# Optimization experiments

Measured on AMD Instinct MI355X. Metric: run time of the kernel, lower is better.

Reference implementation:

```python
import jax, jax.numpy as jnp
import numpy as np

B, N, D = 8, 2048, 128

def setup_inputs() -> dict:
    key = jax.random.key(0)
    k1, k2, k3 = jax.random.split(key, 3)
    embeddings = jax.random.normal(k1, (B, N, D), dtype=jnp.float32)
    cost_matrix = jax.random.uniform(k2, (B, N, N), dtype=jnp.float32)
    W = jax.random.normal(k3, (D, 2 * D), dtype=jnp.float32) * (1.0 / np.sqrt(2 * D))
    b = jnp.zeros((D,), dtype=jnp.float32)
    return {"embeddings": embeddings, "cost_matrix": cost_matrix, "W": W, "b": b}

def reference(embeddings, cost_matrix, W, b):
    # degree[b,j] = number of nonzero entries in row j of cost_matrix
    degree = (cost_matrix != 0).astype(embeddings.dtype).sum(axis=-1)  # [B,N]
    # sum_neighbors[b,j,d] = sum_i embeddings[b,i,d] * cost_matrix[b,i,j]
    # (algebraic rewrite of the O(B*N*N*D) broadcast-multiply-reduce)
    sum_neighbors = jnp.einsum('bij,bid->bjd', cost_matrix, embeddings)
    sum_neighbors = sum_neighbors / degree[..., None]
    concatenated = jnp.concatenate([embeddings, sum_neighbors], axis=-1)  # [B,N,2D]
    return jax.nn.relu(jnp.einsum('bnf,df->bnd', concatenated, W) + b)
```

## Files before the change

kernel.cpp:

```cpp
#include <hip/hip_runtime.h>
#include <stdint.h>

#define B_ 8
#define N_ 2048
#define D_ 128
#define KS_ 4
#define KT_ 8
#define PS_ ((size_t)B_ * N_ * D_)

typedef unsigned short u16;
typedef unsigned int u32;
using f32x4 = __attribute__((ext_vector_type(4))) float;
using bf16x8 = __attribute__((ext_vector_type(8))) short;
using u16x8 = __attribute__((ext_vector_type(8))) u16;

__device__ inline u16 f2bf(float x) {
  u32 u = __float_as_uint(x);
  return (u16)((u + 0x7FFFu + ((u >> 16) & 1u)) >> 16);
}
__device__ inline float bf2f(u16 h) { return __uint_as_float((u32)h << 16); }

__global__ __launch_bounds__(256) void prep_et_kernel(const float* __restrict__ E,
                                                      u16* __restrict__ ET) {
  __shared__ float Els[64][132];
  const int blk = blockIdx.x;
  const int b = blk >> 5;
  const int i0 = (blk & 31) * 64;
  const int t = threadIdx.x;
  const float* Eb = E + ((size_t)b * N_ + i0) * D_;
#pragma unroll
  for (int s = 0; s < 8; ++s) {
    const int r = (t >> 5) + 8 * s;
    const int c = t & 31;
    f32x4 v = *(const f32x4*)(Eb + r * D_ + c * 4);
#pragma unroll
    for (int e = 0; e < 4; ++e) Els[r][c * 4 + e] = v[e];
  }
  __syncthreads();
  u16* ETb = ET + (size_t)b * D_ * N_;
#pragma unroll
  for (int s = 0; s < 4; ++s) {
    const int d = (t >> 3) + 32 * s;
    const int g = t & 7;
    u16x8 pk;
#pragma unroll
    for (int e = 0; e < 8; ++e) pk[e] = f2bf(Els[g * 8 + e][d]);
    *(u16x8*)(ETb + (size_t)d * N_ + i0 + g * 8) = pk;
  }
}

__global__ __launch_bounds__(256) void gemm_kernel(const float* __restrict__ C,
                                                   const u16* __restrict__ ET,
                                                   u16* __restrict__ Sp,
                                                   int* __restrict__ deg) {
  __shared__ __align__(16) u16 Asw[64 * 64];
  __shared__ __align__(16) u16 Bsw[128 * 64];
  const int phys = blockIdx.x;
  const int orig = (phys & 7) * 128 + (phys >> 3);
  const int b = orig >> 7;
  const int ks = (orig >> 5) & 3;
  const int jt = orig & 31;
  const int j0 = jt * 64;
  const int t = threadIdx.x;
  const int lane = t & 63;
  const int wave = t >> 6;
  const int wm = wave >> 1, wn = wave & 1;
  const int lm = lane & 15, lh = lane >> 4;

  const float* Cb = C + (size_t)b * N_ * N_;
  const u16* ETb = ET + (size_t)b * D_ * N_;
  u16* Sb = Sp + (size_t)ks * PS_ + ((size_t)b * N_ + j0) * D_;
  int* degb = deg + b * N_;

  f32x4 acc[2][4];
#pragma unroll
  for (int i = 0; i < 2; ++i)
#pragma unroll
    for (int j = 0; j < 4; ++j) acc[i][j] = (f32x4)0.0f;

  const int aRow = t >> 4, aCol = t & 15;
  const int bG = t & 7;
  const int kbase = ks * (N_ / KS_);

  f32x4 av[4];
  u16x8 bv[4];
#pragma unroll
  for (int s = 0; s < 4; ++s)
    av[s] = *(const f32x4*)(Cb + (size_t)(kbase + aRow + 16 * s) * N_ + j0 + aCol * 4);
#pragma unroll
  for (int s = 0; s < 4; ++s) {
    const int d = (t >> 3) + 32 * s;
    bv[s] = *(const u16x8*)(ETb + (size_t)d * N_ + kbase + bG * 8);
  }

#pragma unroll
  for (int kt = 0; kt < KT_; ++kt) {
    const int i0 = kbase + kt * 64;
#pragma unroll
    for (int s = 0; s < 4; ++s) {
      const int d = (t >> 3) + 32 * s;
      const int swz = (d ^ (d >> 3)) & 7;
      *(u16x8*)&Bsw[d * 64 + ((bG ^ swz) << 3)] = bv[s];
    }
#pragma unroll
    for (int s = 0; s < 4; ++s) {
      const int i = aRow + 16 * s;
      f32x4 v = av[s];
      int cnt = (v[0] != 0.0f) + (v[1] != 0.0f) + (v[2] != 0.0f) + (v[3] != 0.0f);
      cnt += __shfl_xor(cnt, 1);
      cnt += __shfl_xor(cnt, 2);
      cnt += __shfl_xor(cnt, 4);
      cnt += __shfl_xor(cnt, 8);
      if ((lane & 15) == 0) atomicAdd(&degb[i0 + i], cnt);
#pragma unroll
      for (int e = 0; e < 4; ++e) {
        const int jl = aCol * 4 + e;
        const int swz = (jl ^ (jl >> 3)) & 7;
        Asw[jl * 64 + (i ^ (swz << 3))] = f2bf(v[e]);
      }
    }
    if (kt + 1 < KT_) {
      const int i0n = i0 + 64;
#pragma unroll
      for (int s = 0; s < 4; ++s)
        av[s] = *(const f32x4*)(Cb + (size_t)(i0n + aRow + 16 * s) * N_ + j0 + aCol * 4);
#pragma unroll
      for (int s = 0; s < 4; ++s) {
        const int d = (t >> 3) + 32 * s;
        bv[s] = *(const u16x8*)(ETb + (size_t)d * N_ + i0n + bG * 8);
      }
    }
    asm volatile("s_waitcnt lgkmcnt(0)" ::: "memory");
    __builtin_amdgcn_sched_barrier(0);
    __builtin_amdgcn_s_barrier();
    __builtin_amdgcn_sched_barrier(0);
    bf16x8 af[2][2], bfr[4][2];
#pragma unroll
    for (int fm = 0; fm < 2; ++fm) {
      const int jl = wm * 32 + fm * 16 + lm;
      const int swz = (jl ^ (jl >> 3)) & 7;
#pragma unroll
      for (int kf = 0; kf < 2; ++kf) {
        const int K8 = kf * 32 + lh * 8;
        af[fm][kf] = *(const bf16x8*)&Asw[jl * 64 + (K8 ^ (swz << 3))];
      }
    }
#pragma unroll
    for (int fn = 0; fn < 4; ++fn) {
      const int nl = wn * 64 + fn * 16 + lm;
      const int swz = (nl ^ (nl >> 3)) & 7;
#pragma unroll
      for (int kf = 0; kf < 2; ++kf) {
        const int K8 = kf * 32 + lh * 8;
        bfr[fn][kf] = *(const bf16x8*)&Bsw[nl * 64 + (K8 ^ (swz << 3))];
      }
    }
#pragma unroll
    for (int kf = 0; kf < 2; ++kf)
#pragma unroll
      for (int fm = 0; fm < 2; ++fm)
#pragma unroll
        for (int fn = 0; fn < 4; ++fn)
          acc[fm][fn] = __builtin_amdgcn_mfma_f32_16x16x32_bf16(
              af[fm][kf], bfr[fn][kf], acc[fm][fn], 0, 0, 0);
    __builtin_amdgcn_sched_barrier(0);
    __builtin_amdgcn_s_barrier();
    __builtin_amdgcn_sched_barrier(0);
  }
#pragma unroll
  for (int fm = 0; fm < 2; ++fm)
#pragma unroll
    for (int fn = 0; fn < 4; ++fn)
#pragma unroll
      for (int r = 0; r < 4; ++r) {
        const int row = wm * 32 + fm * 16 + lh * 4 + r;
        const int col = wn * 64 + fn * 16 + lm;
        Sb[(size_t)row * D_ + col] = f2bf(acc[fm][fn][r]);
      }
}

__global__ __launch_bounds__(256) void out_kernel(const float* __restrict__ E,
                                                  const u16* __restrict__ Sp,
                                                  const int* __restrict__ deg,
                                                  const float* __restrict__ W,
                                                  const float* __restrict__ bias,
                                                  float* __restrict__ out) {
  __shared__ __align__(16) u16 Wls[128 * 256];
  __shared__ __align__(16) u16 Als[32 * 256];
  const int r0 = blockIdx.x * 32;
  const int t = threadIdx.x;
  const int lane = t & 63;
  const int wave = t >> 6;
  const int lm = lane & 15, lh = lane >> 4;

  {
    const int d = t >> 1;
    const int swz = (d ^ (d >> 3)) & 7;
    const float* Wd = W + d * 256 + (t & 1) * 128;
    const int k8base = (t & 1) * 16;
#pragma unroll
    for (int s = 0; s < 16; ++s) {
      f32x4 v0 = *(const f32x4*)(Wd + s * 8);
      f32x4 v1 = *(const f32x4*)(Wd + s * 8 + 4);
      u16x8 pk;
#pragma unroll
      for (int e = 0; e < 4; ++e) { pk[e] = f2bf(v0[e]); pk[4 + e] = f2bf(v1[e]); }
      *(u16x8*)&Wls[d * 256 + (((k8base + s) ^ swz) << 3)] = pk;
    }
  }
  {
    const int r = t >> 3;
    const int g = t & 7;
    const int swz = (r ^ (r >> 3)) & 7;
    const float idg = 1.0f / (float)deg[r0 + r];
    const float* Er = E + (size_t)(r0 + r) * D_;
#pragma unroll
    for (int h = 0; h < 2; ++h) {
      const int k8 = g + 8 * h;
      f32x4 v0 = *(const f32x4*)(Er + k8 * 8);
      f32x4 v1 = *(const f32x4*)(Er + k8 * 8 + 4);
      u16x8 pk;
#pragma unroll
      for (int e = 0; e < 4; ++e) { pk[e] = f2bf(v0[e]); pk[4 + e] = f2bf(v1[e]); }
      *(u16x8*)&Als[r * 256 + ((k8 ^ swz) << 3)] = pk;
    }
    const size_t off = (size_t)(r0 + r) * D_;
#pragma unroll
    for (int h = 0; h < 2; ++h) {
      const int kq = g + 8 * h;
      u16x8 p0 = *(const u16x8*)(Sp + 0 * PS_ + off + kq * 8);
      u16x8 p1 = *(const u16x8*)(Sp + 1 * PS_ + off + kq * 8);
      u16x8 p2 = *(const u16x8*)(Sp + 2 * PS_ + off + kq * 8);
      u16x8 p3 = *(const u16x8*)(Sp + 3 * PS_ + off + kq * 8);
      u16x8 pk;
#pragma unroll
      for (int e = 0; e < 8; ++e) {
        float s = (bf2f(p0[e]) + bf2f(p1[e])) + (bf2f(p2[e]) + bf2f(p3[e]));
        pk[e] = f2bf(s * idg);
      }
      const int k8 = 16 + kq;
      *(u16x8*)&Als[r * 256 + ((k8 ^ swz) << 3)] = pk;
    }
  }
  __syncthreads();
  f32x4 acc[2][2];
#pragma unroll
  for (int i = 0; i < 2; ++i)
#pragma unroll
    for (int j = 0; j < 2; ++j) acc[i][j] = (f32x4)0.0f;
  const int dbase = wave * 32;
#pragma unroll
  for (int kf = 0; kf < 8; ++kf) {
    bf16x8 af[2], bfr[2];
#pragma unroll
    for (int fm = 0; fm < 2; ++fm) {
      const int r = fm * 16 + lm;
      const int swz = (r ^ (r >> 3)) & 7;
      af[fm] = *(const bf16x8*)&Als[r * 256 + (((kf * 4 + lh) ^ swz) << 3)];
    }
#pragma unroll
    for (int fn = 0; fn < 2; ++fn) {
      const int d = dbase + fn * 16 + lm;
      const int swz = (d ^ (d >> 3)) & 7;
      bfr[fn] = *(const bf16x8*)&Wls[d * 256 + (((kf * 4 + lh) ^ swz) << 3)];
    }
#pragma unroll
    for (int fm = 0; fm < 2; ++fm)
#pragma unroll
      for (int fn = 0; fn < 2; ++fn)
        acc[fm][fn] = __builtin_amdgcn_mfma_f32_16x16x32_bf16(af[fm], bfr[fn],
                                                              acc[fm][fn], 0, 0, 0);
  }
  float bb[2] = {bias[dbase + lm], bias[dbase + 16 + lm]};
#pragma unroll
  for (int fm = 0; fm < 2; ++fm)
#pragma unroll
    for (int fn = 0; fn < 2; ++fn)
#pragma unroll
      for (int r = 0; r < 4; ++r) {
        const int row = r0 + fm * 16 + lh * 4 + r;
        const int d = dbase + fn * 16 + lm;
        float x = acc[fm][fn][r] + bb[fn];
        out[(size_t)row * D_ + d] = x > 0.0f ? x : 0.0f;
      }
}

extern "C" void kernel_launch(void* const* d_in, const int* in_sizes, int n_in,
                              void* d_out, int out_size, void* d_ws, size_t ws_size,
                              hipStream_t stream) {
  (void)in_sizes; (void)n_in; (void)out_size; (void)ws_size;
  const float* E = (const float*)d_in[0];
  const float* C = (const float*)d_in[1];
  const float* W = (const float*)d_in[2];
  const float* bias = (const float*)d_in[3];
  float* out = (float*)d_out;

  int* deg = (int*)d_ws;
  u16* ET = (u16*)((char*)d_ws + 65536);
  u16* Sp = (u16*)((char*)d_ws + 65536 + 4194304);

  hipMemsetAsync(deg, 0, B_ * N_ * sizeof(int), stream);
  hipLaunchKernelGGL(prep_et_kernel, dim3(256), dim3(256), 0, stream, E, ET);
  hipLaunchKernelGGL(gemm_kernel, dim3(1024), dim3(256), 0, stream, C, ET, Sp, deg);
  hipLaunchKernelGGL(out_kernel, dim3(512), dim3(256), 0, stream, E, Sp, deg, W, bias, out);
}
```

Measured before the change: 230.6 us.

## Double-buffer GEMM with direct global-to-LDS loads of pre-swizzled E tiles

Prep kernel now writes embeddings as pre-swizzled bf16 tile images so the GEMM can copy them straight into LDS with global_load_lds, double-buffered against MFMA work. The K split drops from 4 to 2, halving the grid and the partial-sum traffic the output kernel reduces. W is converted to swizzled bf16 once by a single-block kernel and copied into LDS directly instead of each output block converting it. This trades less occupancy and parallelism in the GEMM for fewer global round trips and better load/compute overlap.

```diff
diff --git a/kernel.cpp b/kernel.cpp
--- a/kernel.cpp
+++ b/kernel.cpp
@@ -4,8 +4,9 @@
 #define B_ 8
 #define N_ 2048
 #define D_ 128
-#define KS_ 4
-#define KT_ 8
+#define NT_ 32
+#define KT_ 16
+#define TILE_BYTES 16384
 #define PS_ ((size_t)B_ * N_ * D_)
 
 typedef unsigned short u16;
@@ -20,45 +21,69 @@
 }
 __device__ inline float bf2f(u16 h) { return __uint_as_float((u32)h << 16); }
 
+__device__ inline void glds16(const void* g, void* l) {
+  __builtin_amdgcn_global_load_lds((const __attribute__((address_space(1))) void*)g,
+                                   (__attribute__((address_space(3))) void*)l, 16, 0, 0);
+}
+
 __global__ __launch_bounds__(256) void prep_et_kernel(const float* __restrict__ E,
-                                                      u16* __restrict__ ET) {
+                                                      u16* __restrict__ ETsw) {
   __shared__ float Els[64][132];
   const int blk = blockIdx.x;
   const int b = blk >> 5;
-  const int i0 = (blk & 31) * 64;
+  const int g = blk & 31;
   const int t = threadIdx.x;
-  const float* Eb = E + ((size_t)b * N_ + i0) * D_;
+  const float* Eb = E + ((size_t)b * N_ + g * 64) * D_;
 #pragma unroll
   for (int s = 0; s < 8; ++s) {
-    const int r = (t >> 5) + 8 * s;
-    const int c = t & 31;
-    f32x4 v = *(const f32x4*)(Eb + r * D_ + c * 4);
-#pragma unroll
-    for (int e = 0; e < 4; ++e) Els[r][c * 4 + e] = v[e];
+    const int f4 = t + 256 * s;
+    const int r = f4 >> 5;
+    const int c4 = f4 & 31;
+    f32x4 v = *(const f32x4*)(Eb + (size_t)r * D_ + c4 * 4);
+#pragma unroll
+    for (int e = 0; e < 4; ++e) Els[r][c4 * 4 + e] = v[e];
   }
   __syncthreads();
-  u16* ETb = ET + (size_t)b * D_ * N_;
-#pragma unroll
-  for (int s = 0; s < 4; ++s) {
-    const int d = (t >> 3) + 32 * s;
-    const int g = t & 7;
+  u16* img = ETsw + ((size_t)b * NT_ + g) * (TILE_BYTES / 2);
+  const int d = t >> 1;
+  const int swz = (d ^ (d >> 3)) & 7;
+#pragma unroll
+  for (int gg = 0; gg < 4; ++gg) {
+    const int grp = (t & 1) * 4 + gg;
     u16x8 pk;
 #pragma unroll
-    for (int e = 0; e < 8; ++e) pk[e] = f2bf(Els[g * 8 + e][d]);
-    *(u16x8*)(ETb + (size_t)d * N_ + i0 + g * 8) = pk;
+    for (int e = 0; e < 8; ++e) pk[e] = f2bf(Els[grp * 8 + e][d]);
+    *(u16x8*)(img + d * 64 + ((grp ^ swz) << 3)) = pk;
+  }
+}
+
+__global__ __launch_bounds__(256) void prep_w_kernel(const float* __restrict__ W,
+                                                     u16* __restrict__ Wsw) {
+  const int t = threadIdx.x;
+  const int d = t >> 1;
+  const int swz = (d ^ (d >> 3)) & 7;
+#pragma unroll
+  for (int s = 0; s < 16; ++s) {
+    const int k8 = (t & 1) * 16 + s;
+    f32x4 v0 = *(const f32x4*)(W + d * 256 + k8 * 8);
+    f32x4 v1 = *(const f32x4*)(W + d * 256 + k8 * 8 + 4);
+    u16x8 pk;
+#pragma unroll
+    for (int e = 0; e < 4; ++e) { pk[e] = f2bf(v0[e]); pk[4 + e] = f2bf(v1[e]); }
+    *(u16x8*)(Wsw + d * 256 + ((k8 ^ swz) << 3)) = pk;
   }
 }
 
 __global__ __launch_bounds__(256) void gemm_kernel(const float* __restrict__ C,
-                                                   const u16* __restrict__ ET,
+                                                   const u16* __restrict__ ETsw,
                                                    u16* __restrict__ Sp,
                                                    int* __restrict__ deg) {
-  __shared__ __align__(16) u16 Asw[64 * 64];
-  __shared__ __align__(16) u16 Bsw[128 * 64];
+  __shared__ __align__(16) u16 Asw[2][64 * 64];
+  __shared__ __align__(16) u16 Bsw[2][128 * 64];
   const int phys = blockIdx.x;
-  const int orig = (phys & 7) * 128 + (phys >> 3);
-  const int b = orig >> 7;
-  const int ks = (orig >> 5) & 3;
+  const int orig = (phys & 7) * 64 + (phys >> 3);
+  const int b = orig >> 6;
+  const int ks = (orig >> 5) & 1;
   const int jt = orig & 31;
   const int j0 = jt * 64;
   const int t = threadIdx.x;
@@ -66,107 +91,106 @@
   const int wave = t >> 6;
   const int wm = wave >> 1, wn = wave & 1;
   const int lm = lane & 15, lh = lane >> 4;
+  const int aRow = t >> 4, aCol = t & 15;
 
   const float* Cb = C + (size_t)b * N_ * N_;
-  const u16* ETb = ET + (size_t)b * D_ * N_;
+  const char* Eimg = (const char*)(ETsw + (size_t)b * NT_ * (TILE_BYTES / 2));
+  int* degb = deg + b * N_;
+  const int g0 = ks * KT_;
+
+  f32x4 acc[2][4];
+#pragma unroll
+  for (int i = 0; i < 2; ++i)
+#pragma unroll
+    for (int j = 0; j < 4; ++j) acc[i][j] = (f32x4)0.0f;
+  f32x4 av[4];
+
+#define ISSUE_B(gi, buf)                                                          \
+  {                                                                               \
+    _Pragma("unroll") for (int s = 0; s < 4; ++s) {                               \
+      const int chunk = s * 4 + wave;                                             \
+      glds16(Eimg + (size_t)(gi)*TILE_BYTES + chunk * 1024 + lane * 16,           \
+             (char*)&Bsw[buf][0] + chunk * 1024);                                 \
+    }                                                                             \
+  }
+#define LOAD_A(gi)                                                                \
+  {                                                                               \
+    _Pragma("unroll") for (int s = 0; s < 4; ++s) av[s] =                         \
+        *(const f32x4*)(Cb + (size_t)((gi)*64 + aRow + 16 * s) * N_ + j0 + aCol * 4); \
+  }
+#define WRITE_A(gi, buf)                                                          \
+  {                                                                               \
+    _Pragma("unroll") for (int s = 0; s < 4; ++s) {                               \
+      const int i = aRow + 16 * s;                                                \
+      f32x4 v = av[s];                                                            \
+      int cnt = (v[0] != 0.0f) + (v[1] != 0.0f) + (v[2] != 0.0f) + (v[3] != 0.0f);\
+      cnt += __shfl_xor(cnt, 1);                                                  \
+      cnt += __shfl_xor(cnt, 2);                                                  \
+      cnt += __shfl_xor(cnt, 4);                                                  \
+      cnt += __shfl_xor(cnt, 8);                                                  \
+      if ((lane & 15) == 0) atomicAdd(&degb[(gi)*64 + i], cnt);                   \
+      _Pragma("unroll") for (int e = 0; e < 4; ++e) {                             \
+        const int jl = aCol * 4 + e;                                              \
+        const int sz = (jl ^ (jl >> 3)) & 7;                                      \
+        Asw[buf][jl * 64 + (i ^ (sz << 3))] = f2bf(v[e]);                         \
+      }                                                                           \
+    }                                                                             \
+  }
+#define MFMA_PHASE(buf)                                                           \
+  {                                                                               \
+    bf16x8 af[2][2], bfr[4][2];                                                   \
+    _Pragma("unroll") for (int fm = 0; fm < 2; ++fm) {                            \
+      const int jl = wm * 32 + fm * 16 + lm;                                      \
+      const int sz = (jl ^ (jl >> 3)) & 7;                                        \
+      _Pragma("unroll") for (int kf = 0; kf < 2; ++kf) {                          \
+        const int K8 = kf * 32 + lh * 8;                                          \
+        af[fm][kf] = *(const bf16x8*)&Asw[buf][jl * 64 + (K8 ^ (sz << 3))];       \
+      }                                                                           \
+    }                                                                             \
+    _Pragma("unroll") for (int fn = 0; fn < 4; ++fn) {                            \
+      const int nl = wn * 64 + fn * 16 + lm;                                      \
+      const int sz = (nl ^ (nl >> 3)) & 7;                                        \
+      _Pragma("unroll") for (int kf = 0; kf < 2; ++kf) {                          \
+        const int K8 = kf * 32 + lh * 8;                                          \
+        bfr[fn][kf] = *(const bf16x8*)&Bsw[buf][nl * 64 + (K8 ^ (sz << 3))];      \
+      }                                                                           \
+    }                                                                             \
+    _Pragma("unroll") for (int kf = 0; kf < 2; ++kf)                              \
+        _Pragma("unroll") for (int fm = 0; fm < 2; ++fm)                          \
+        _Pragma("unroll") for (int fn = 0; fn < 4; ++fn) acc[fm][fn] =            \
+        __builtin_amdgcn_mfma_f32_16x16x32_bf16(af[fm][kf], bfr[fn][kf],          \
+                                                acc[fm][fn], 0, 0, 0);            \
+  }
+
+  ISSUE_B(g0, 0);
+  LOAD_A(g0);
+  WRITE_A(g0, 0);
+  LOAD_A(g0 + 1);
+  asm volatile("s_waitcnt lgkmcnt(0)" ::: "memory");
+  __builtin_amdgcn_sched_barrier(0);
+  __builtin_amdgcn_s_barrier();
+  __builtin_amdgcn_sched_barrier(0);
+
+  int cur = 0;
+  for (int kt = 0; kt < KT_ - 1; ++kt) {
+    ISSUE_B(g0 + kt + 1, cur ^ 1);
+    __builtin_amdgcn_sched_barrier(0);
+    MFMA_PHASE(cur);
+    __builtin_amdgcn_sched_barrier(0);
+    WRITE_A(g0 + kt + 1, cur ^ 1);
+    __builtin_amdgcn_sched_barrier(0);
+    if (kt < KT_ - 2) LOAD_A(g0 + kt + 2);
+    __builtin_amdgcn_sched_barrier(0);
+    asm volatile("s_waitcnt vmcnt(8)" ::: "memory");
+    asm volatile("s_waitcnt lgkmcnt(0)" ::: "memory");
+    __builtin_amdgcn_sched_barrier(0);
+    __builtin_amdgcn_s_barrier();
+    __builtin_amdgcn_sched_barrier(0);
+    cur ^= 1;
+  }
+  MFMA_PHASE(cur);
+
   u16* Sb = Sp + (size_t)ks * PS_ + ((size_t)b * N_ + j0) * D_;
-  int* degb = deg + b * N_;
-
-  f32x4 acc[2][4];
-#pragma unroll
-  for (int i = 0; i < 2; ++i)
-#pragma unroll
-    for (int j = 0; j < 4; ++j) acc[i][j] = (f32x4)0.0f;
-
-  const int aRow = t >> 4, aCol = t & 15;
-  const int bG = t & 7;
-  const int kbase = ks * (N_ / KS_);
-
-  f32x4 av[4];
-  u16x8 bv[4];
-#pragma unroll
-  for (int s = 0; s < 4; ++s)
-    av[s] = *(const f32x4*)(Cb + (size_t)(kbase + aRow + 16 * s) * N_ + j0 + aCol * 4);
-#pragma unroll
-  for (int s = 0; s < 4; ++s) {
-    const int d = (t >> 3) + 32 * s;
-    bv[s] = *(const u16x8*)(ETb + (size_t)d * N_ + kbase + bG * 8);
-  }
-
-#pragma unroll
-  for (int kt = 0; kt < KT_; ++kt) {
-    const int i0 = kbase + kt * 64;
-#pragma unroll
-    for (int s = 0; s < 4; ++s) {
-      const int d = (t >> 3) + 32 * s;
-      const int swz = (d ^ (d >> 3)) & 7;
-      *(u16x8*)&Bsw[d * 64 + ((bG ^ swz) << 3)] = bv[s];
-    }
-#pragma unroll
-    for (int s = 0; s < 4; ++s) {
-      const int i = aRow + 16 * s;
-      f32x4 v = av[s];
-      int cnt = (v[0] != 0.0f) + (v[1] != 0.0f) + (v[2] != 0.0f) + (v[3] != 0.0f);
-      cnt += __shfl_xor(cnt, 1);
-      cnt += __shfl_xor(cnt, 2);
-      cnt += __shfl_xor(cnt, 4);
-      cnt += __shfl_xor(cnt, 8);
-      if ((lane & 15) == 0) atomicAdd(&degb[i0 + i], cnt);
-#pragma unroll
-      for (int e = 0; e < 4; ++e) {
-        const int jl = aCol * 4 + e;
-        const int swz = (jl ^ (jl >> 3)) & 7;
-        Asw[jl * 64 + (i ^ (swz << 3))] = f2bf(v[e]);
-      }
-    }
-    if (kt + 1 < KT_) {
-      const int i0n = i0 + 64;
-#pragma unroll
-      for (int s = 0; s < 4; ++s)
-        av[s] = *(const f32x4*)(Cb + (size_t)(i0n + aRow + 16 * s) * N_ + j0 + aCol * 4);
-#pragma unroll
-      for (int s = 0; s < 4; ++s) {
-        const int d = (t >> 3) + 32 * s;
-        bv[s] = *(const u16x8*)(ETb + (size_t)d * N_ + i0n + bG * 8);
-      }
-    }
-    asm volatile("s_waitcnt lgkmcnt(0)" ::: "memory");
-    __builtin_amdgcn_sched_barrier(0);
-    __builtin_amdgcn_s_barrier();
-    __builtin_amdgcn_sched_barrier(0);
-    bf16x8 af[2][2], bfr[4][2];
-#pragma unroll
-    for (int fm = 0; fm < 2; ++fm) {
-      const int jl = wm * 32 + fm * 16 + lm;
-      const int swz = (jl ^ (jl >> 3)) & 7;
-#pragma unroll
-      for (int kf = 0; kf < 2; ++kf) {
-        const int K8 = kf * 32 + lh * 8;
-        af[fm][kf] = *(const bf16x8*)&Asw[jl * 64 + (K8 ^ (swz << 3))];
-      }
-    }
-#pragma unroll
-    for (int fn = 0; fn < 4; ++fn) {
-      const int nl = wn * 64 + fn * 16 + lm;
-      const int swz = (nl ^ (nl >> 3)) & 7;
-#pragma unroll
-      for (int kf = 0; kf < 2; ++kf) {
-        const int K8 = kf * 32 + lh * 8;
-        bfr[fn][kf] = *(const bf16x8*)&Bsw[nl * 64 + (K8 ^ (swz << 3))];
-      }
-    }
-#pragma unroll
-    for (int kf = 0; kf < 2; ++kf)
-#pragma unroll
-      for (int fm = 0; fm < 2; ++fm)
-#pragma unroll
-        for (int fn = 0; fn < 4; ++fn)
-          acc[fm][fn] = __builtin_amdgcn_mfma_f32_16x16x32_bf16(
-              af[fm][kf], bfr[fn][kf], acc[fm][fn], 0, 0, 0);
-    __builtin_amdgcn_sched_barrier(0);
-    __builtin_amdgcn_s_barrier();
-    __builtin_amdgcn_sched_barrier(0);
-  }
 #pragma unroll
   for (int fm = 0; fm < 2; ++fm)
 #pragma unroll
@@ -177,12 +201,16 @@
         const int col = wn * 64 + fn * 16 + lm;
         Sb[(size_t)row * D_ + col] = f2bf(acc[fm][fn][r]);
       }
+#undef ISSUE_B
+#undef LOAD_A
+#undef WRITE_A
+#undef MFMA_PHASE
 }
 
 __global__ __launch_bounds__(256) void out_kernel(const float* __restrict__ E,
                                                   const u16* __restrict__ Sp,
                                                   const int* __restrict__ deg,
-                                                  const float* __restrict__ W,
+                                                  const u16* __restrict__ Wsw,
                                                   const float* __restrict__ bias,
                                                   float* __restrict__ out) {
   __shared__ __align__(16) u16 Wls[128 * 256];
@@ -193,56 +221,38 @@
   const int wave = t >> 6;
   const int lm = lane & 15, lh = lane >> 4;
 
-  {
-    const int d = t >> 1;
-    const int swz = (d ^ (d >> 3)) & 7;
-    const float* Wd = W + d * 256 + (t & 1) * 128;
-    const int k8base = (t & 1) * 16;
-#pragma unroll
-    for (int s = 0; s < 16; ++s) {
-      f32x4 v0 = *(const f32x4*)(Wd + s * 8);
-      f32x4 v1 = *(const f32x4*)(Wd + s * 8 + 4);
-      u16x8 pk;
-#pragma unroll
-      for (int e = 0; e < 4; ++e) { pk[e] = f2bf(v0[e]); pk[4 + e] = f2bf(v1[e]); }
-      *(u16x8*)&Wls[d * 256 + (((k8base + s) ^ swz) << 3)] = pk;
-    }
-  }
-  {
-    const int r = t >> 3;
-    const int g = t & 7;
-    const int swz = (r ^ (r >> 3)) & 7;
-    const float idg = 1.0f / (float)deg[r0 + r];
-    const float* Er = E + (size_t)(r0 + r) * D_;
-#pragma unroll
-    for (int h = 0; h < 2; ++h) {
-      const int k8 = g + 8 * h;
-      f32x4 v0 = *(const f32x4*)(Er + k8 * 8);
-      f32x4 v1 = *(const f32x4*)(Er + k8 * 8 + 4);
-      u16x8 pk;
-#pragma unroll
-      for (int e = 0; e < 4; ++e) { pk[e] = f2bf(v0[e]); pk[4 + e] = f2bf(v1[e]); }
-      *(u16x8*)&Als[r * 256 + ((k8 ^ swz) << 3)] = pk;
-    }
-    const size_t off = (size_t)(r0 + r) * D_;
-#pragma unroll
-    for (int h = 0; h < 2; ++h) {
-      const int kq = g + 8 * h;
-      u16x8 p0 = *(const u16x8*)(Sp + 0 * PS_ + off + kq * 8);
-      u16x8 p1 = *(const u16x8*)(Sp + 1 * PS_ + off + kq * 8);
-      u16x8 p2 = *(const u16x8*)(Sp + 2 * PS_ + off + kq * 8);
-      u16x8 p3 = *(const u16x8*)(Sp + 3 * PS_ + off + kq * 8);
-      u16x8 pk;
-#pragma unroll
-      for (int e = 0; e < 8; ++e) {
-        float s = (bf2f(p0[e]) + bf2f(p1[e])) + (bf2f(p2[e]) + bf2f(p3[e]));
-        pk[e] = f2bf(s * idg);
-      }
-      const int k8 = 16 + kq;
-      *(u16x8*)&Als[r * 256 + ((k8 ^ swz) << 3)] = pk;
-    }
+#pragma unroll
+  for (int s = 0; s < 16; ++s) {
+    const int chunk = s * 4 + wave;
+    glds16((const char*)Wsw + chunk * 1024 + lane * 16, (char*)Wls + chunk * 1024);
+  }
+  const int r = t >> 3, gq = t & 7;
+  const int swzr = (r ^ (r >> 3)) & 7;
+  const float idg = 1.0f / (float)deg[r0 + r];
+  const float* Er = E + (size_t)(r0 + r) * D_;
+#pragma unroll
+  for (int h = 0; h < 2; ++h) {
+    const int k8 = gq + 8 * h;
+    f32x4 v0 = *(const f32x4*)(Er + k8 * 8);
+    f32x4 v1 = *(const f32x4*)(Er + k8 * 8 + 4);
+    u16x8 pk;
+#pragma unroll
+    for (int e = 0; e < 4; ++e) { pk[e] = f2bf(v0[e]); pk[4 + e] = f2bf(v1[e]); }
+    *(u16x8*)&Als[r * 256 + ((k8 ^ swzr) << 3)] = pk;
+  }
+  const size_t off = (size_t)(r0 + r) * D_;
+#pragma unroll
+  for (int h = 0; h < 2; ++h) {
+    const int kq = gq + 8 * h;
+    u16x8 p0 = *(const u16x8*)(Sp + off + kq * 8);
+    u16x8 p1 = *(const u16x8*)(Sp + PS_ + off + kq * 8);
+    u16x8 pk;
+#pragma unroll
+    for (int e = 0; e < 8; ++e) pk[e] = f2bf((bf2f(p0[e]) + bf2f(p1[e])) * idg);
+    *(u16x8*)&Als[r * 256 + (((16 + kq) ^ swzr) << 3)] = pk;
   }
   __syncthreads();
+
   f32x4 acc[2][2];
 #pragma unroll
   for (int i = 0; i < 2; ++i)
@@ -254,15 +264,15 @@
     bf16x8 af[2], bfr[2];
 #pragma unroll
     for (int fm = 0; fm < 2; ++fm) {
-      const int r = fm * 16 + lm;
-      const int swz = (r ^ (r >> 3)) & 7;
-      af[fm] = *(const bf16x8*)&Als[r * 256 + (((kf * 4 + lh) ^ swz) << 3)];
+      const int rr = fm * 16 + lm;
+      const int sz = (rr ^ (rr >> 3)) & 7;
+      af[fm] = *(const bf16x8*)&Als[rr * 256 + (((kf * 4 + lh) ^ sz) << 3)];
     }
 #pragma unroll
     for (int fn = 0; fn < 2; ++fn) {
       const int d = dbase + fn * 16 + lm;
-      const int swz = (d ^ (d >> 3)) & 7;
-      bfr[fn] = *(const bf16x8*)&Wls[d * 256 + (((kf * 4 + lh) ^ swz) << 3)];
+      const int sz = (d ^ (d >> 3)) & 7;
+      bfr[fn] = *(const bf16x8*)&Wls[d * 256 + (((kf * 4 + lh) ^ sz) << 3)];
     }
 #pragma unroll
     for (int fm = 0; fm < 2; ++fm)
@@ -277,10 +287,10 @@
 #pragma unroll
     for (int fn = 0; fn < 2; ++fn)
 #pragma unroll
-      for (int r = 0; r < 4; ++r) {
-        const int row = r0 + fm * 16 + lh * 4 + r;
+      for (int rr = 0; rr < 4; ++rr) {
+        const int row = r0 + fm * 16 + lh * 4 + rr;
         const int d = dbase + fn * 16 + lm;
-        float x = acc[fm][fn][r] + bb[fn];
+        float x = acc[fm][fn][rr] + bb[fn];
         out[(size_t)row * D_ + d] = x > 0.0f ? x : 0.0f;
       }
 }
@@ -295,12 +305,15 @@
   const float* bias = (const float*)d_in[3];
   float* out = (float*)d_out;
 
-  int* deg = (int*)d_ws;
-  u16* ET = (u16*)((char*)d_ws + 65536);
-  u16* Sp = (u16*)((char*)d_ws + 65536 + 4194304);
+  char* ws = (char*)d_ws;
+  int* deg = (int*)ws;
+  u16* ETsw = (u16*)(ws + 65536);
+  u16* Wsw = (u16*)(ws + 65536 + 4194304);
+  u16* Sp = (u16*)(ws + 65536 + 4194304 + 65536);
 
   hipMemsetAsync(deg, 0, B_ * N_ * sizeof(int), stream);
-  hipLaunchKernelGGL(prep_et_kernel, dim3(256), dim3(256), 0, stream, E, ET);
-  hipLaunchKernelGGL(gemm_kernel, dim3(1024), dim3(256), 0, stream, C, ET, Sp, deg);
-  hipLaunchKernelGGL(out_kernel, dim3(512), dim3(256), 0, stream, E, Sp, deg, W, bias, out);
-}
+  hipLaunchKernelGGL(prep_et_kernel, dim3(256), dim3(256), 0, stream, E, ETsw);
+  hipLaunchKernelGGL(prep_w_kernel, dim3(1), dim3(256), 0, stream, W, Wsw);
+  hipLaunchKernelGGL(gemm_kernel, dim3(512), dim3(256), 0, stream, C, ETsw, Sp, deg);
+  hipLaunchKernelGGL(out_kernel, dim3(512), dim3(256), 0, stream, E, Sp, deg, Wsw, bias, out);
+}
```

Result: no change. 229.0 us (-0.7%).
